# Kernel tuning notes

Hardware: AMD Instinct MI355X
Metric: run time of the kernel (lower is better)

## Reference

```python
import jax, jax.numpy as jnp
import numpy as np

B, S, D, H, L = 64, 512, 512, 512, 2


def gru_cell(x, h, Wih, Whh, bih, bhh):
    # PyTorch GRUCell math: gates ordered (r, z, n)
    gi = x @ Wih.T + bih          # [B, 3H]
    gh = h @ Whh.T + bhh          # [B, 3H]
    ir, iz, i_n = jnp.split(gi, 3, axis=-1)
    hr, hz, h_n = jnp.split(gh, 3, axis=-1)
    r = jax.nn.sigmoid(ir + hr)
    z = jax.nn.sigmoid(iz + hz)
    n = jnp.tanh(i_n + r * h_n)
    return (1.0 - z) * n + z * h


def setup_inputs() -> dict:
    key = jax.random.key(0)
    ks = jax.random.split(key, 12)
    s = 0.05
    inp = {
        "input": jax.random.normal(ks[0], (B, S, D), jnp.float32),
        "encoder_h": jax.random.normal(ks[1], (L, B, 2 * H), jnp.float32),
        # stacked per-layer GRUCell params (input_size == hidden_size so layer dims match)
        "Wih_f": jax.random.normal(ks[2], (L, 3 * H, D), jnp.float32) * s,
        "Whh_f": jax.random.normal(ks[3], (L, 3 * H, H), jnp.float32) * s,
        "bih_f": jax.random.normal(ks[4], (L, 3 * H), jnp.float32) * s,
        "bhh_f": jax.random.normal(ks[5], (L, 3 * H), jnp.float32) * s,
        "Wih_b": jax.random.normal(ks[6], (L, 3 * H, D), jnp.float32) * s,
        "Whh_b": jax.random.normal(ks[7], (L, 3 * H, H), jnp.float32) * s,
        "bih_b": jax.random.normal(ks[8], (L, 3 * H), jnp.float32) * s,
        "bhh_b": jax.random.normal(ks[9], (L, 3 * H), jnp.float32) * s,
    }
    return inp


def reference(input, encoder_h, Wih_f, Whh_f, bih_f, bhh_f, Wih_b, Whh_b, bih_b, bhh_b):
    n_layers = Wih_f.shape[0]
    hidden = Whh_f.shape[-1]
    h_f0 = encoder_h[:, :, :hidden]   # [L, B, H]
    h_b0 = encoder_h[:, :, hidden:]   # [L, B, H]
    xs_f = jnp.swapaxes(input, 0, 1)  # [S, B, D]
    xs_b = jnp.flip(xs_f, axis=0)     # reversed sequence

    def step(carry, xt):
        h_f, h_b = carry
        x_f, x_b = xt
        hf_new, hb_new = [], []
        for j in range(n_layers):
            x_f = gru_cell(x_f, h_f[j], Wih_f[j], Whh_f[j], bih_f[j], bhh_f[j])
            x_b = gru_cell(x_b, h_b[j], Wih_b[j], Whh_b[j], bih_b[j], bhh_b[j])
            hf_new.append(x_f)
            hb_new.append(x_b)
        return (jnp.stack(hf_new), jnp.stack(hb_new)), (x_f, x_b)

    (h_f, h_b), (out_f, out_b) = jax.lax.scan(step, (h_f0, h_b0), (xs_f, xs_b))
    out_f = jnp.swapaxes(out_f, 0, 1)                  # [B, S, H]
    out_b = jnp.flip(jnp.swapaxes(out_b, 0, 1), axis=1)  # un-reverse in time
    out = jnp.concatenate([out_f, out_b], axis=-1)      # [B, S, 2H]
    h = jnp.concatenate([h_f, h_b], axis=-1)            # [L, B, 2H]
    return out, h
```

## Files before the change

### kernel.cpp

```cpp
#include <hip/hip_runtime.h>

constexpr int BATCH = 64;
constexpr int SEQ   = 512;
constexpr int DIN   = 512;
constexpr int HID   = 512;
constexpr int LAY   = 2;
constexpr int G3    = 3 * HID;
constexpr int KPAD  = 522;

typedef __attribute__((ext_vector_type(8))) short bf16x8;
typedef __attribute__((ext_vector_type(4))) float f32x4;
typedef unsigned short u16;
typedef unsigned int   u32;
typedef unsigned long long u64;

__device__ __forceinline__ u16 f2bf(float f) {
  union { float f; u32 u; } v; v.f = f;
  return (u16)((v.u + 0x7fffu + ((v.u >> 16) & 1u)) >> 16);
}

__device__ __forceinline__ u64 ld_agent_u64(const u16* p) {
  return __hip_atomic_load((const u64*)p, __ATOMIC_RELAXED, __HIP_MEMORY_SCOPE_AGENT);
}
__device__ __forceinline__ bf16x8 ld_frag_agent(const u16* p) {
  union { u64 q[2]; bf16x8 f; } u;
  u.q[0] = ld_agent_u64(p);
  u.q[1] = ld_agent_u64(p + 4);
  return u.f;
}
__device__ __forceinline__ void st_agent_u16(u16* p, u16 v) {
  __hip_atomic_store(p, v, __ATOMIC_RELAXED, __HIP_MEMORY_SCOPE_AGENT);
}
__device__ __forceinline__ void st_agent_u32(u32* p, u32 v) {
  __hip_atomic_store(p, v, __ATOMIC_RELAXED, __HIP_MEMORY_SCOPE_AGENT);
}

__device__ __forceinline__ void poll_ge(const u32* flags, u32 target) {
  const int idx = threadIdx.x & 31;
  for (;;) {
    u32 v = __hip_atomic_load(flags + idx, __ATOMIC_RELAXED, __HIP_MEMORY_SCOPE_AGENT);
    #pragma unroll
    for (int off = 16; off >= 1; off >>= 1) {
      u32 o = (u32)__shfl_xor((int)v, off, 64);
      v = v < o ? v : o;
    }
    if (v >= target) break;
    __builtin_amdgcn_s_sleep(1);
  }
  __asm__ volatile("" ::: "memory");
}

struct Params {
  const float* input;
  const float* enc_h;
  const float* Wih[2];
  const float* Whh[2];
  const float* bih[2];
  const float* bhh[2];
  float* out;
  u16* xin;
  u16* wih;
  u16* whh;
  u16* out0;
  u16* hbf;
  u32* flags;
};

__global__ __launch_bounds__(256) void convert_kernel(Params p) {
  const int gtid = blockIdx.x * 256 + threadIdx.x;
  const int nthr = gridDim.x * 256;
  for (int i = gtid; i < BATCH * SEQ * DIN; i += nthr) p.xin[i] = f2bf(p.input[i]);
  for (int d = 0; d < 2; ++d) {
    const float* s1 = p.Wih[d];
    u16* d1 = p.wih + (size_t)d * LAY * G3 * DIN;
    for (int i = gtid; i < LAY * G3 * DIN; i += nthr) d1[i] = f2bf(s1[i]);
    const float* s2 = p.Whh[d];
    u16* d2 = p.whh + (size_t)d * LAY * G3 * HID;
    for (int i = gtid; i < LAY * G3 * HID; i += nthr) d2[i] = f2bf(s2[i]);
  }
  if (gtid < LAY * 2 * 32) p.flags[gtid] = 0;
}

__global__ __launch_bounds__(256, 1) void recur_all(Params p) {
  const int wg    = blockIdx.x;
  const int layer = wg >> 6;
  const int cwg   = wg & 63;
  const int dir   = cwg & 1;
  const int slice = cwg >> 1;
  const int j0    = slice * 16;
  const int wave  = threadIdx.x >> 6;
  const int lane  = threadIdx.x & 63;
  const int lq = lane >> 4, ln = lane & 15;
  const int j = j0 + ln;

  __shared__ u16 lwhh[3][16][KPAD];
  {
    const u16* whh = p.whh + ((size_t)dir * LAY + layer) * G3 * HID;
    for (int idx = threadIdx.x; idx < 3 * 16 * 64; idx += 256) {
      const int k8 = idx & 63, row = idx >> 6;
      const int g = row >> 4, jj = row & 15;
      *(bf16x8*)&lwhh[g][jj][k8 * 8] =
          *(const bf16x8*)(whh + (size_t)(g * HID + j0 + jj) * HID + k8 * 8);
    }
  }

  u16* hbL = p.hbf + (size_t)layer * 2 * 2 * BATCH * HID;
  u16* hb[2] = { hbL + (size_t)dir * BATCH * HID,
                 hbL + (size_t)(2 + dir) * BATCH * HID };

  const u16* wih = p.wih + ((size_t)dir * LAY + layer) * G3 * DIN;
  const u16* bri[3];
  #pragma unroll
  for (int g = 0; g < 3; ++g) bri[g] = wih + (size_t)(g * HID + j) * DIN;

  const float* bih = p.bih[dir] + (size_t)layer * G3;
  const float* bhh = p.bhh[dir] + (size_t)layer * G3;
  const float b_r  = bih[j] + bhh[j];
  const float b_z  = bih[HID + j] + bhh[HID + j];
  const float bi_n = bih[2 * HID + j];
  const float bh_n = bhh[2 * HID + j];

  float hreg[4];
  #pragma unroll
  for (int i = 0; i < 4; ++i) {
    const int m = wave * 16 + lq * 4 + i;
    hreg[i] = p.enc_h[((size_t)layer * BATCH + m) * (2 * HID) + (size_t)dir * HID + j];
    st_agent_u16(&hb[0][(size_t)m * HID + j], f2bf(hreg[i]));
  }

  u32* fown  = p.flags + (size_t)(layer * 2 + dir) * 32;
  u32* fdep  = p.flags + (size_t)dir * 32;
  u32* fslot = fown + slice;

  __threadfence_block();
  __syncthreads();
  if (threadIdx.x == 0) st_agent_u32(fslot, 1);

  const int am = wave * 16 + ln;
  float* hsec = p.out + (size_t)BATCH * SEQ * 2 * HID;

  f32x4 accx[3];
  if (layer == 1) poll_ge(fdep, 2);
  {
    const u16* ax = (layer == 0)
        ? p.xin + ((size_t)am * SEQ + (dir ? SEQ - 1 : 0)) * DIN
        : p.out0 + ((size_t)dir * SEQ * BATCH + am) * HID;
    accx[0] = f32x4{0, 0, 0, 0}; accx[1] = accx[0]; accx[2] = accx[0];
    #pragma unroll 4
    for (int k0 = 0; k0 < 512; k0 += 32) {
      const int koff = k0 + lq * 8;
      const bf16x8 a_x = (layer == 0) ? *(const bf16x8*)(ax + koff)
                                      : ld_frag_agent(ax + koff);
      #pragma unroll
      for (int g = 0; g < 3; ++g)
        accx[g] = __builtin_amdgcn_mfma_f32_16x16x32_bf16(
            a_x, *(const bf16x8*)(bri[g] + koff), accx[g], 0, 0, 0);
    }
  }
  poll_ge(fown, 1);

  for (int t = 0; t < SEQ; ++t) {
    const u16* ah = hb[t & 1] + (size_t)am * HID;
    f32x4 acch[3] = {};
    #pragma unroll 4
    for (int k0 = 0; k0 < 512; k0 += 32) {
      const int koff = k0 + lq * 8;
      const bf16x8 a_h = ld_frag_agent(ah + koff);
      #pragma unroll
      for (int g = 0; g < 3; ++g)
        acch[g] = __builtin_amdgcn_mfma_f32_16x16x32_bf16(
            a_h, *(const bf16x8*)&lwhh[g][ln][koff], acch[g], 0, 0, 0);
    }

    u16* hwrite = hb[(t + 1) & 1];
    #pragma unroll
    for (int i = 0; i < 4; ++i) {
      const int m = wave * 16 + lq * 4 + i;
      const float r = 1.f / (1.f + __expf(-(accx[0][i] + acch[0][i] + b_r)));
      const float z = 1.f / (1.f + __expf(-(accx[1][i] + acch[1][i] + b_z)));
      const float n = tanhf(accx[2][i] + bi_n + r * (acch[2][i] + bh_n));
      const float hnew = (1.f - z) * n + z * hreg[i];
      hreg[i] = hnew;
      if (t + 1 < SEQ) st_agent_u16(&hwrite[(size_t)m * HID + j], f2bf(hnew));
      if (layer == 0) {
        st_agent_u16(&p.out0[(((size_t)dir * SEQ + t) * BATCH + m) * HID + j], f2bf(hnew));
      } else {
        const int tt = dir ? (SEQ - 1 - t) : t;
        p.out[((size_t)m * SEQ + tt) * (2 * HID) + (size_t)dir * HID + j] = hnew;
      }
      if (t == SEQ - 1)
        hsec[((size_t)layer * BATCH + m) * (2 * HID) + (size_t)dir * HID + j] = hnew;
    }

    __threadfence_block();
    __syncthreads();
    if (threadIdx.x == 0) st_agent_u32(fslot, (u32)(t + 2));

    if (t + 1 < SEQ) {
      if (layer == 1) poll_ge(fdep, (u32)(t + 3));
      const int tn = t + 1;
      const u16* ax = (layer == 0)
          ? p.xin + ((size_t)am * SEQ + (dir ? SEQ - 1 - tn : tn)) * DIN
          : p.out0 + (((size_t)dir * SEQ + tn) * BATCH + am) * HID;
      accx[0] = f32x4{0, 0, 0, 0}; accx[1] = accx[0]; accx[2] = accx[0];
      #pragma unroll 4
      for (int k0 = 0; k0 < 512; k0 += 32) {
        const int koff = k0 + lq * 8;
        const bf16x8 a_x = (layer == 0) ? *(const bf16x8*)(ax + koff)
                                        : ld_frag_agent(ax + koff);
        #pragma unroll
        for (int g = 0; g < 3; ++g)
          accx[g] = __builtin_amdgcn_mfma_f32_16x16x32_bf16(
              a_x, *(const bf16x8*)(bri[g] + koff), accx[g], 0, 0, 0);
      }
      poll_ge(fown, (u32)(t + 2));
    }
  }
}

extern "C" void kernel_launch(void* const* d_in, const int* in_sizes, int n_in,
                              void* d_out, int out_size, void* d_ws, size_t ws_size,
                              hipStream_t stream) {
  Params p;
  p.input  = (const float*)d_in[0];
  p.enc_h  = (const float*)d_in[1];
  p.Wih[0] = (const float*)d_in[2];
  p.Whh[0] = (const float*)d_in[3];
  p.bih[0] = (const float*)d_in[4];
  p.bhh[0] = (const float*)d_in[5];
  p.Wih[1] = (const float*)d_in[6];
  p.Whh[1] = (const float*)d_in[7];
  p.bih[1] = (const float*)d_in[8];
  p.bhh[1] = (const float*)d_in[9];
  p.out = (float*)d_out;

  uintptr_t base = (uintptr_t)d_ws;
  size_t off = 0;
  auto take = [&](size_t bytes) -> void* {
    void* r = (void*)(base + off);
    off += (bytes + 255) & ~(size_t)255;
    return r;
  };
  p.xin   = (u16*)take((size_t)BATCH * SEQ * DIN * 2);
  p.wih   = (u16*)take((size_t)2 * LAY * G3 * DIN * 2);
  p.whh   = (u16*)take((size_t)2 * LAY * G3 * HID * 2);
  p.out0  = (u16*)take((size_t)2 * SEQ * BATCH * HID * 2);
  p.hbf   = (u16*)take((size_t)LAY * 2 * 2 * BATCH * HID * 2);
  p.flags = (u32*)take((size_t)LAY * 2 * 32 * 4);
  if (off > ws_size) return;

  convert_kernel<<<dim3(2048), dim3(256), 0, stream>>>(p);
  recur_all<<<dim3(128), dim3(256), 0, stream>>>(p);
}
```

Before: 8.067 ms.

## Halve workgroups with wider hidden slices and switch to atomic-counter barrier

Each workgroup now handles 32 hidden units with 512 threads (8 waves split over batch and output tiles), so 64 workgroups run instead of 128. Per-slice flag arrays with shuffle-min polling are replaced by one atomic fetch-add counter per cell, polled by a single wave and then a block barrier. The recurrent h fragments are preloaded into registers right after the input projection, and the LDS weight tile uses an XOR swizzle instead of padding. The goal is fewer participants in each cross-workgroup sync and lower per-step latency. The cost is higher register pressure, atomic contention on one counter, and an extra __syncthreads per step.

```diff
diff --git a/kernel.cpp b/kernel.cpp
--- a/kernel.cpp
+++ b/kernel.cpp
@@ -6,7 +6,11 @@
 constexpr int HID   = 512;
 constexpr int LAY   = 2;
 constexpr int G3    = 3 * HID;
-constexpr int KPAD  = 522;
+
+constexpr int NSLICE = 16;
+constexpr int WSLICE = 32;
+constexpr int NTHR   = 512;
+constexpr int CNTPAD = 1024;
 
 typedef __attribute__((ext_vector_type(8))) short bf16x8;
 typedef __attribute__((ext_vector_type(4))) float f32x4;
@@ -31,19 +35,10 @@
 __device__ __forceinline__ void st_agent_u16(u16* p, u16 v) {
   __hip_atomic_store(p, v, __ATOMIC_RELAXED, __HIP_MEMORY_SCOPE_AGENT);
 }
-__device__ __forceinline__ void st_agent_u32(u32* p, u32 v) {
-  __hip_atomic_store(p, v, __ATOMIC_RELAXED, __HIP_MEMORY_SCOPE_AGENT);
-}
-
-__device__ __forceinline__ void poll_ge(const u32* flags, u32 target) {
-  const int idx = threadIdx.x & 31;
+
+__device__ __forceinline__ void poll1(const u32* c, u32 target) {
   for (;;) {
-    u32 v = __hip_atomic_load(flags + idx, __ATOMIC_RELAXED, __HIP_MEMORY_SCOPE_AGENT);
-    #pragma unroll
-    for (int off = 16; off >= 1; off >>= 1) {
-      u32 o = (u32)__shfl_xor((int)v, off, 64);
-      v = v < o ? v : o;
-    }
+    u32 v = __hip_atomic_load(c, __ATOMIC_RELAXED, __HIP_MEMORY_SCOPE_AGENT);
     if (v >= target) break;
     __builtin_amdgcn_s_sleep(1);
   }
@@ -63,7 +58,7 @@
   u16* whh;
   u16* out0;
   u16* hbf;
-  u32* flags;
+  u32* cnt;
 };
 
 __global__ __launch_bounds__(256) void convert_kernel(Params p) {
@@ -78,35 +73,39 @@
     u16* d2 = p.whh + (size_t)d * LAY * G3 * HID;
     for (int i = gtid; i < LAY * G3 * HID; i += nthr) d2[i] = f2bf(s2[i]);
   }
-  if (gtid < LAY * 2 * 32) p.flags[gtid] = 0;
-}
-
-__global__ __launch_bounds__(256, 1) void recur_all(Params p) {
+  if (gtid < 4 * CNTPAD) p.cnt[gtid] = 0;
+}
+
+__global__ __launch_bounds__(NTHR, 1) void recur_all(Params p) {
   const int wg    = blockIdx.x;
-  const int layer = wg >> 6;
-  const int cwg   = wg & 63;
-  const int dir   = cwg & 1;
-  const int slice = cwg >> 1;
-  const int j0    = slice * 16;
-  const int wave  = threadIdx.x >> 6;
-  const int lane  = threadIdx.x & 63;
+  const int cell  = wg & 3;
+  const int layer = cell >> 1;
+  const int dir   = cell & 1;
+  const int slice = wg >> 2;
+  const int j0    = slice * WSLICE;
+
+  const int wave = threadIdx.x >> 6;
+  const int lane = threadIdx.x & 63;
   const int lq = lane >> 4, ln = lane & 15;
-  const int j = j0 + ln;
-
-  __shared__ u16 lwhh[3][16][KPAD];
+  const int mt = wave & 3, nt = wave >> 2;
+  const int am = mt * 16 + ln;
+  const int rr = nt * 16 + ln;
+  const int j  = j0 + rr;
+
+  __shared__ u16 lwhh[3][WSLICE][512];
   {
     const u16* whh = p.whh + ((size_t)dir * LAY + layer) * G3 * HID;
-    for (int idx = threadIdx.x; idx < 3 * 16 * 64; idx += 256) {
+    for (int idx = threadIdx.x; idx < 3 * WSLICE * 64; idx += NTHR) {
       const int k8 = idx & 63, row = idx >> 6;
-      const int g = row >> 4, jj = row & 15;
-      *(bf16x8*)&lwhh[g][jj][k8 * 8] =
+      const int g = row >> 5, jj = row & 31;
+      *(bf16x8*)&lwhh[g][jj][(k8 ^ (jj & 7)) * 8] =
           *(const bf16x8*)(whh + (size_t)(g * HID + j0 + jj) * HID + k8 * 8);
     }
   }
 
   u16* hbL = p.hbf + (size_t)layer * 2 * 2 * BATCH * HID;
-  u16* hb[2] = { hbL + (size_t)dir * BATCH * HID,
-                 hbL + (size_t)(2 + dir) * BATCH * HID };
+  u16* hb0 = hbL + (size_t)dir * BATCH * HID;
+  u16* hb1 = hbL + (size_t)(2 + dir) * BATCH * HID;
 
   const u16* wih = p.wih + ((size_t)dir * LAY + layer) * G3 * DIN;
   const u16* bri[3];
@@ -123,59 +122,70 @@
   float hreg[4];
   #pragma unroll
   for (int i = 0; i < 4; ++i) {
-    const int m = wave * 16 + lq * 4 + i;
+    const int m = mt * 16 + lq * 4 + i;
     hreg[i] = p.enc_h[((size_t)layer * BATCH + m) * (2 * HID) + (size_t)dir * HID + j];
-    st_agent_u16(&hb[0][(size_t)m * HID + j], f2bf(hreg[i]));
-  }
-
-  u32* fown  = p.flags + (size_t)(layer * 2 + dir) * 32;
-  u32* fdep  = p.flags + (size_t)dir * 32;
-  u32* fslot = fown + slice;
+    st_agent_u16(&hb0[(size_t)m * HID + j], f2bf(hreg[i]));
+  }
+
+  u32* own = p.cnt + (size_t)cell * CNTPAD;
+  u32* dep = p.cnt + (size_t)dir  * CNTPAD;
 
   __threadfence_block();
   __syncthreads();
-  if (threadIdx.x == 0) st_agent_u32(fslot, 1);
-
-  const int am = wave * 16 + ln;
+  if (threadIdx.x == 0)
+    __hip_atomic_fetch_add(own, 1u, __ATOMIC_RELAXED, __HIP_MEMORY_SCOPE_AGENT);
+
   float* hsec = p.out + (size_t)BATCH * SEQ * 2 * HID;
 
-  f32x4 accx[3];
-  if (layer == 1) poll_ge(fdep, 2);
+  bf16x8 fr[16];
+  f32x4  accx[3];
+
+  if (layer == 1) { if (wave == 0) poll1(dep, 2 * NSLICE); __syncthreads(); }
   {
     const u16* ax = (layer == 0)
         ? p.xin + ((size_t)am * SEQ + (dir ? SEQ - 1 : 0)) * DIN
         : p.out0 + ((size_t)dir * SEQ * BATCH + am) * HID;
-    accx[0] = f32x4{0, 0, 0, 0}; accx[1] = accx[0]; accx[2] = accx[0];
-    #pragma unroll 4
-    for (int k0 = 0; k0 < 512; k0 += 32) {
-      const int koff = k0 + lq * 8;
-      const bf16x8 a_x = (layer == 0) ? *(const bf16x8*)(ax + koff)
-                                      : ld_frag_agent(ax + koff);
-      #pragma unroll
-      for (int g = 0; g < 3; ++g)
-        accx[g] = __builtin_amdgcn_mfma_f32_16x16x32_bf16(
-            a_x, *(const bf16x8*)(bri[g] + koff), accx[g], 0, 0, 0);
-    }
-  }
-  poll_ge(fown, 1);
+    if (layer == 0) {
+      #pragma unroll
+      for (int kk = 0; kk < 16; ++kk) fr[kk] = *(const bf16x8*)(ax + kk * 32 + lq * 8);
+    } else {
+      #pragma unroll
+      for (int kk = 0; kk < 16; ++kk) fr[kk] = ld_frag_agent(ax + kk * 32 + lq * 8);
+    }
+  }
+  if (wave == 0) poll1(own, NSLICE);
+  __syncthreads();
+  accx[0] = f32x4{0.f, 0.f, 0.f, 0.f}; accx[1] = accx[0]; accx[2] = accx[0];
+  #pragma unroll
+  for (int kk = 0; kk < 16; ++kk) {
+    #pragma unroll
+    for (int g = 0; g < 3; ++g)
+      accx[g] = __builtin_amdgcn_mfma_f32_16x16x32_bf16(
+          fr[kk], *(const bf16x8*)(bri[g] + kk * 32 + lq * 8), accx[g], 0, 0, 0);
+  }
+  {
+    const u16* ah = hb0 + (size_t)am * HID;
+    #pragma unroll
+    for (int kk = 0; kk < 16; ++kk) fr[kk] = ld_frag_agent(ah + kk * 32 + lq * 8);
+  }
 
   for (int t = 0; t < SEQ; ++t) {
-    const u16* ah = hb[t & 1] + (size_t)am * HID;
-    f32x4 acch[3] = {};
-    #pragma unroll 4
-    for (int k0 = 0; k0 < 512; k0 += 32) {
-      const int koff = k0 + lq * 8;
-      const bf16x8 a_h = ld_frag_agent(ah + koff);
+    f32x4 acch[3];
+    acch[0] = f32x4{0.f, 0.f, 0.f, 0.f}; acch[1] = acch[0]; acch[2] = acch[0];
+    #pragma unroll
+    for (int kk = 0; kk < 16; ++kk) {
       #pragma unroll
       for (int g = 0; g < 3; ++g)
         acch[g] = __builtin_amdgcn_mfma_f32_16x16x32_bf16(
-            a_h, *(const bf16x8*)&lwhh[g][ln][koff], acch[g], 0, 0, 0);
-    }
-
-    u16* hwrite = hb[(t + 1) & 1];
+            fr[kk],
+            *(const bf16x8*)&lwhh[g][rr][(((kk << 2) + lq) ^ (rr & 7)) * 8],
+            acch[g], 0, 0, 0);
+    }
+
+    u16* hwrite = ((t + 1) & 1) ? hb1 : hb0;
     #pragma unroll
     for (int i = 0; i < 4; ++i) {
-      const int m = wave * 16 + lq * 4 + i;
+      const int m = mt * 16 + lq * 4 + i;
       const float r = 1.f / (1.f + __expf(-(accx[0][i] + acch[0][i] + b_r)));
       const float z = 1.f / (1.f + __expf(-(accx[1][i] + acch[1][i] + b_z)));
       const float n = tanhf(accx[2][i] + bi_n + r * (acch[2][i] + bh_n));
@@ -194,26 +204,35 @@
 
     __threadfence_block();
     __syncthreads();
-    if (threadIdx.x == 0) st_agent_u32(fslot, (u32)(t + 2));
+    if (threadIdx.x == 0)
+      __hip_atomic_fetch_add(own, 1u, __ATOMIC_RELAXED, __HIP_MEMORY_SCOPE_AGENT);
 
     if (t + 1 < SEQ) {
-      if (layer == 1) poll_ge(fdep, (u32)(t + 3));
       const int tn = t + 1;
+      if (layer == 1) { if (wave == 0) poll1(dep, (u32)(NSLICE * (tn + 2))); __syncthreads(); }
       const u16* ax = (layer == 0)
           ? p.xin + ((size_t)am * SEQ + (dir ? SEQ - 1 - tn : tn)) * DIN
           : p.out0 + (((size_t)dir * SEQ + tn) * BATCH + am) * HID;
-      accx[0] = f32x4{0, 0, 0, 0}; accx[1] = accx[0]; accx[2] = accx[0];
-      #pragma unroll 4
-      for (int k0 = 0; k0 < 512; k0 += 32) {
-        const int koff = k0 + lq * 8;
-        const bf16x8 a_x = (layer == 0) ? *(const bf16x8*)(ax + koff)
-                                        : ld_frag_agent(ax + koff);
+      if (layer == 0) {
+        #pragma unroll
+        for (int kk = 0; kk < 16; ++kk) fr[kk] = *(const bf16x8*)(ax + kk * 32 + lq * 8);
+      } else {
+        #pragma unroll
+        for (int kk = 0; kk < 16; ++kk) fr[kk] = ld_frag_agent(ax + kk * 32 + lq * 8);
+      }
+      if (wave == 0) poll1(own, (u32)(NSLICE * (t + 2)));
+      __syncthreads();
+      accx[0] = f32x4{0.f, 0.f, 0.f, 0.f}; accx[1] = accx[0]; accx[2] = accx[0];
+      #pragma unroll
+      for (int kk = 0; kk < 16; ++kk) {
         #pragma unroll
         for (int g = 0; g < 3; ++g)
           accx[g] = __builtin_amdgcn_mfma_f32_16x16x32_bf16(
-              a_x, *(const bf16x8*)(bri[g] + koff), accx[g], 0, 0, 0);
+              fr[kk], *(const bf16x8*)(bri[g] + kk * 32 + lq * 8), accx[g], 0, 0, 0);
       }
-      poll_ge(fown, (u32)(t + 2));
+      const u16* ah = ((tn & 1) ? hb1 : hb0) + (size_t)am * HID;
+      #pragma unroll
+      for (int kk = 0; kk < 16; ++kk) fr[kk] = ld_frag_agent(ah + kk * 32 + lq * 8);
     }
   }
 }
@@ -246,9 +265,9 @@
   p.whh   = (u16*)take((size_t)2 * LAY * G3 * HID * 2);
   p.out0  = (u16*)take((size_t)2 * SEQ * BATCH * HID * 2);
   p.hbf   = (u16*)take((size_t)LAY * 2 * 2 * BATCH * HID * 2);
-  p.flags = (u32*)take((size_t)LAY * 2 * 32 * 4);
+  p.cnt   = (u32*)take((size_t)4 * CNTPAD * 4);
   if (off > ws_size) return;
 
   convert_kernel<<<dim3(2048), dim3(256), 0, stream>>>(p);
-  recur_all<<<dim3(128), dim3(256), 0, stream>>>(p);
-}
+  recur_all<<<dim3(64), dim3(NTHR), 0, stream>>>(p);
+}
```

New measurement: 13.43 ms. 1.66x slower.

## Fuse both GRU layers into one wavefront-skewed workgroup per slice

Applied to the files above, without the earlier changes.

Each workgroup now computes both layers for its hidden slice and direction. Layer 1 runs one timestep behind layer 0, so one step's layer-0 hidden-state fragment serves both the layer-0 recurrent GEMM and the layer-1 input GEMM. This removes the separate layer-1 workgroups, the out0 staging buffer and the cross-layer flag polling, and halves the grid from 128 to 64 workgroups. In exchange each workgroup does roughly twice the serial MFMA work per step with half the parallelism, and holds both layers' Whh slices in LDS.

```diff
diff --git a/kernel.cpp b/kernel.cpp
--- a/kernel.cpp
+++ b/kernel.cpp
@@ -61,7 +61,6 @@
   u16* xin;
   u16* wih;
   u16* whh;
-  u16* out0;
   u16* hbf;
   u32* flags;
 };
@@ -78,142 +77,182 @@
     u16* d2 = p.whh + (size_t)d * LAY * G3 * HID;
     for (int i = gtid; i < LAY * G3 * HID; i += nthr) d2[i] = f2bf(s2[i]);
   }
-  if (gtid < LAY * 2 * 32) p.flags[gtid] = 0;
+  if (gtid < 2 * 32) p.flags[gtid] = 0;
 }
 
 __global__ __launch_bounds__(256, 1) void recur_all(Params p) {
   const int wg    = blockIdx.x;
-  const int layer = wg >> 6;
-  const int cwg   = wg & 63;
-  const int dir   = cwg & 1;
-  const int slice = cwg >> 1;
+  const int dir   = wg & 1;
+  const int slice = wg >> 1;
   const int j0    = slice * 16;
   const int wave  = threadIdx.x >> 6;
   const int lane  = threadIdx.x & 63;
   const int lq = lane >> 4, ln = lane & 15;
-  const int j = j0 + ln;
-
-  __shared__ u16 lwhh[3][16][KPAD];
+  const int j  = j0 + ln;
+  const int am = wave * 16 + ln;
+
+  __shared__ u16 lwhh[LAY][3][16][KPAD];
   {
-    const u16* whh = p.whh + ((size_t)dir * LAY + layer) * G3 * HID;
-    for (int idx = threadIdx.x; idx < 3 * 16 * 64; idx += 256) {
+    const u16* whh = p.whh + (size_t)dir * LAY * G3 * HID;
+    for (int idx = threadIdx.x; idx < LAY * 3 * 16 * 64; idx += 256) {
       const int k8 = idx & 63, row = idx >> 6;
-      const int g = row >> 4, jj = row & 15;
-      *(bf16x8*)&lwhh[g][jj][k8 * 8] =
-          *(const bf16x8*)(whh + (size_t)(g * HID + j0 + jj) * HID + k8 * 8);
-    }
-  }
-
-  u16* hbL = p.hbf + (size_t)layer * 2 * 2 * BATCH * HID;
-  u16* hb[2] = { hbL + (size_t)dir * BATCH * HID,
-                 hbL + (size_t)(2 + dir) * BATCH * HID };
-
-  const u16* wih = p.wih + ((size_t)dir * LAY + layer) * G3 * DIN;
-  const u16* bri[3];
+      const int lay = row >= 48;
+      const int rem = row - lay * 48;
+      const int g = rem >> 4, jj = rem & 15;
+      *(bf16x8*)&lwhh[lay][g][jj][k8 * 8] =
+          *(const bf16x8*)(whh + ((size_t)lay * G3 + (size_t)(g * HID + j0 + jj)) * HID + k8 * 8);
+    }
+  }
+
+  u16* h0b[2], * h1b[2];
   #pragma unroll
-  for (int g = 0; g < 3; ++g) bri[g] = wih + (size_t)(g * HID + j) * DIN;
-
-  const float* bih = p.bih[dir] + (size_t)layer * G3;
-  const float* bhh = p.bhh[dir] + (size_t)layer * G3;
-  const float b_r  = bih[j] + bhh[j];
-  const float b_z  = bih[HID + j] + bhh[HID + j];
-  const float bi_n = bih[2 * HID + j];
-  const float bh_n = bhh[2 * HID + j];
-
-  float hreg[4];
+  for (int par = 0; par < 2; ++par) {
+    h0b[par] = p.hbf + ((size_t)(0 * 2 + par) * 2 + dir) * BATCH * HID;
+    h1b[par] = p.hbf + ((size_t)(1 * 2 + par) * 2 + dir) * BATCH * HID;
+  }
+
+  const u16* wih = p.wih + (size_t)dir * LAY * G3 * DIN;
+  const u16* bri0[3];
+  const u16* bri1[3];
+  #pragma unroll
+  for (int g = 0; g < 3; ++g) {
+    bri0[g] = wih + (size_t)(g * HID + j) * DIN;
+    bri1[g] = wih + ((size_t)G3 + (size_t)(g * HID + j)) * DIN;
+  }
+
+  const float* bih0 = p.bih[dir];
+  const float* bhh0 = p.bhh[dir];
+  const float* bih1 = bih0 + G3;
+  const float* bhh1 = bhh0 + G3;
+  const float b0_r  = bih0[j] + bhh0[j];
+  const float b0_z  = bih0[HID + j] + bhh0[HID + j];
+  const float b0_in = bih0[2 * HID + j];
+  const float b0_hn = bhh0[2 * HID + j];
+  const float b1_r  = bih1[j] + bhh1[j];
+  const float b1_z  = bih1[HID + j] + bhh1[HID + j];
+  const float b1_in = bih1[2 * HID + j];
+  const float b1_hn = bhh1[2 * HID + j];
+
+  float hreg0[4], hreg1[4];
   #pragma unroll
   for (int i = 0; i < 4; ++i) {
     const int m = wave * 16 + lq * 4 + i;
-    hreg[i] = p.enc_h[((size_t)layer * BATCH + m) * (2 * HID) + (size_t)dir * HID + j];
-    st_agent_u16(&hb[0][(size_t)m * HID + j], f2bf(hreg[i]));
-  }
-
-  u32* fown  = p.flags + (size_t)(layer * 2 + dir) * 32;
-  u32* fdep  = p.flags + (size_t)dir * 32;
+    hreg0[i] = p.enc_h[(size_t)m * (2 * HID) + (size_t)dir * HID + j];
+    st_agent_u16(&h0b[0][(size_t)m * HID + j], f2bf(hreg0[i]));
+    hreg1[i] = p.enc_h[((size_t)BATCH + m) * (2 * HID) + (size_t)dir * HID + j];
+    st_agent_u16(&h1b[0][(size_t)m * HID + j], f2bf(hreg1[i]));
+  }
+
+  u32* fown  = p.flags + (size_t)dir * 32;
   u32* fslot = fown + slice;
 
   __threadfence_block();
   __syncthreads();
   if (threadIdx.x == 0) st_agent_u32(fslot, 1);
 
-  const int am = wave * 16 + ln;
   float* hsec = p.out + (size_t)BATCH * SEQ * 2 * HID;
 
-  f32x4 accx[3];
-  if (layer == 1) poll_ge(fdep, 2);
+  f32x4 accx0[3];
+  accx0[0] = f32x4{0, 0, 0, 0}; accx0[1] = accx0[0]; accx0[2] = accx0[0];
   {
-    const u16* ax = (layer == 0)
-        ? p.xin + ((size_t)am * SEQ + (dir ? SEQ - 1 : 0)) * DIN
-        : p.out0 + ((size_t)dir * SEQ * BATCH + am) * HID;
-    accx[0] = f32x4{0, 0, 0, 0}; accx[1] = accx[0]; accx[2] = accx[0];
+    const u16* ax = p.xin + ((size_t)am * SEQ + (dir ? SEQ - 1 : 0)) * DIN;
     #pragma unroll 4
     for (int k0 = 0; k0 < 512; k0 += 32) {
       const int koff = k0 + lq * 8;
-      const bf16x8 a_x = (layer == 0) ? *(const bf16x8*)(ax + koff)
-                                      : ld_frag_agent(ax + koff);
-      #pragma unroll
-      for (int g = 0; g < 3; ++g)
-        accx[g] = __builtin_amdgcn_mfma_f32_16x16x32_bf16(
-            a_x, *(const bf16x8*)(bri[g] + koff), accx[g], 0, 0, 0);
+      const bf16x8 a_x = *(const bf16x8*)(ax + koff);
+      #pragma unroll
+      for (int g = 0; g < 3; ++g)
+        accx0[g] = __builtin_amdgcn_mfma_f32_16x16x32_bf16(
+            a_x, *(const bf16x8*)(bri0[g] + koff), accx0[g], 0, 0, 0);
     }
   }
   poll_ge(fown, 1);
 
-  for (int t = 0; t < SEQ; ++t) {
-    const u16* ah = hb[t & 1] + (size_t)am * HID;
-    f32x4 acch[3] = {};
+  for (int i = 0; i <= SEQ; ++i) {
+    const u16* h0r = h0b[i & 1] + (size_t)am * HID;
+    const u16* h1r = h1b[(i + 1) & 1] + (size_t)am * HID;
+    f32x4 acch0[3], accx1[3], acch1[3];
+    acch0[0] = f32x4{0, 0, 0, 0}; acch0[1] = acch0[0]; acch0[2] = acch0[0];
+    accx1[0] = acch0[0]; accx1[1] = acch0[0]; accx1[2] = acch0[0];
+    acch1[0] = acch0[0]; acch1[1] = acch0[0]; acch1[2] = acch0[0];
     #pragma unroll 4
     for (int k0 = 0; k0 < 512; k0 += 32) {
       const int koff = k0 + lq * 8;
-      const bf16x8 a_h = ld_frag_agent(ah + koff);
-      #pragma unroll
-      for (int g = 0; g < 3; ++g)
-        acch[g] = __builtin_amdgcn_mfma_f32_16x16x32_bf16(
-            a_h, *(const bf16x8*)&lwhh[g][ln][koff], acch[g], 0, 0, 0);
-    }
-
-    u16* hwrite = hb[(t + 1) & 1];
-    #pragma unroll
-    for (int i = 0; i < 4; ++i) {
-      const int m = wave * 16 + lq * 4 + i;
-      const float r = 1.f / (1.f + __expf(-(accx[0][i] + acch[0][i] + b_r)));
-      const float z = 1.f / (1.f + __expf(-(accx[1][i] + acch[1][i] + b_z)));
-      const float n = tanhf(accx[2][i] + bi_n + r * (acch[2][i] + bh_n));
-      const float hnew = (1.f - z) * n + z * hreg[i];
-      hreg[i] = hnew;
-      if (t + 1 < SEQ) st_agent_u16(&hwrite[(size_t)m * HID + j], f2bf(hnew));
-      if (layer == 0) {
-        st_agent_u16(&p.out0[(((size_t)dir * SEQ + t) * BATCH + m) * HID + j], f2bf(hnew));
-      } else {
-        const int tt = dir ? (SEQ - 1 - t) : t;
+      const bf16x8 a0 = ld_frag_agent(h0r + koff);
+      #pragma unroll
+      for (int g = 0; g < 3; ++g)
+        acch0[g] = __builtin_amdgcn_mfma_f32_16x16x32_bf16(
+            a0, *(const bf16x8*)&lwhh[0][g][ln][koff], acch0[g], 0, 0, 0);
+      #pragma unroll
+      for (int g = 0; g < 3; ++g)
+        accx1[g] = __builtin_amdgcn_mfma_f32_16x16x32_bf16(
+            a0, *(const bf16x8*)(bri1[g] + koff), accx1[g], 0, 0, 0);
+    }
+    #pragma unroll 4
+    for (int k0 = 0; k0 < 512; k0 += 32) {
+      const int koff = k0 + lq * 8;
+      const bf16x8 a1 = ld_frag_agent(h1r + koff);
+      #pragma unroll
+      for (int g = 0; g < 3; ++g)
+        acch1[g] = __builtin_amdgcn_mfma_f32_16x16x32_bf16(
+            a1, *(const bf16x8*)&lwhh[1][g][ln][koff], acch1[g], 0, 0, 0);
+    }
+
+    if (i < SEQ) {
+      u16* hw = h0b[(i + 1) & 1];
+      #pragma unroll
+      for (int r = 0; r < 4; ++r) {
+        const int m = wave * 16 + lq * 4 + r;
+        const float rg = 1.f / (1.f + __expf(-(accx0[0][r] + acch0[0][r] + b0_r)));
+        const float zg = 1.f / (1.f + __expf(-(accx0[1][r] + acch0[1][r] + b0_z)));
+        const float ng = tanhf(accx0[2][r] + b0_in + rg * (acch0[2][r] + b0_hn));
+        const float hnew = (1.f - zg) * ng + zg * hreg0[r];
+        hreg0[r] = hnew;
+        st_agent_u16(&hw[(size_t)m * HID + j], f2bf(hnew));
+        if (i == SEQ - 1)
+          hsec[(size_t)m * (2 * HID) + (size_t)dir * HID + j] = hnew;
+      }
+    }
+
+    if (i >= 1) {
+      const int t  = i - 1;
+      const int tt = dir ? (SEQ - 1 - t) : t;
+      u16* hw = h1b[i & 1];
+      #pragma unroll
+      for (int r = 0; r < 4; ++r) {
+        const int m = wave * 16 + lq * 4 + r;
+        const float rg = 1.f / (1.f + __expf(-(accx1[0][r] + acch1[0][r] + b1_r)));
+        const float zg = 1.f / (1.f + __expf(-(accx1[1][r] + acch1[1][r] + b1_z)));
+        const float ng = tanhf(accx1[2][r] + b1_in + rg * (acch1[2][r] + b1_hn));
+        const float hnew = (1.f - zg) * ng + zg * hreg1[r];
+        hreg1[r] = hnew;
+        if (i < SEQ) st_agent_u16(&hw[(size_t)m * HID + j], f2bf(hnew));
         p.out[((size_t)m * SEQ + tt) * (2 * HID) + (size_t)dir * HID + j] = hnew;
+        if (i == SEQ)
+          hsec[((size_t)BATCH + m) * (2 * HID) + (size_t)dir * HID + j] = hnew;
       }
-      if (t == SEQ - 1)
-        hsec[((size_t)layer * BATCH + m) * (2 * HID) + (size_t)dir * HID + j] = hnew;
     }
 
     __threadfence_block();
     __syncthreads();
-    if (threadIdx.x == 0) st_agent_u32(fslot, (u32)(t + 2));
-
-    if (t + 1 < SEQ) {
-      if (layer == 1) poll_ge(fdep, (u32)(t + 3));
-      const int tn = t + 1;
-      const u16* ax = (layer == 0)
-          ? p.xin + ((size_t)am * SEQ + (dir ? SEQ - 1 - tn : tn)) * DIN
-          : p.out0 + (((size_t)dir * SEQ + tn) * BATCH + am) * HID;
-      accx[0] = f32x4{0, 0, 0, 0}; accx[1] = accx[0]; accx[2] = accx[0];
-      #pragma unroll 4
-      for (int k0 = 0; k0 < 512; k0 += 32) {
-        const int koff = k0 + lq * 8;
-        const bf16x8 a_x = (layer == 0) ? *(const bf16x8*)(ax + koff)
-                                        : ld_frag_agent(ax + koff);
-        #pragma unroll
-        for (int g = 0; g < 3; ++g)
-          accx[g] = __builtin_amdgcn_mfma_f32_16x16x32_bf16(
-              a_x, *(const bf16x8*)(bri[g] + koff), accx[g], 0, 0, 0);
+    if (threadIdx.x == 0) st_agent_u32(fslot, (u32)(i + 2));
+
+    if (i < SEQ) {
+      if (i + 1 < SEQ) {
+        const int tn = i + 1;
+        const u16* ax = p.xin + ((size_t)am * SEQ + (dir ? SEQ - 1 - tn : tn)) * DIN;
+        accx0[0] = f32x4{0, 0, 0, 0}; accx0[1] = accx0[0]; accx0[2] = accx0[0];
+        #pragma unroll 4
+        for (int k0 = 0; k0 < 512; k0 += 32) {
+          const int koff = k0 + lq * 8;
+          const bf16x8 a_x = *(const bf16x8*)(ax + koff);
+          #pragma unroll
+          for (int g = 0; g < 3; ++g)
+            accx0[g] = __builtin_amdgcn_mfma_f32_16x16x32_bf16(
+                a_x, *(const bf16x8*)(bri0[g] + koff), accx0[g], 0, 0, 0);
+        }
       }
-      poll_ge(fown, (u32)(t + 2));
+      poll_ge(fown, (u32)(i + 2));
     }
   }
 }
@@ -244,11 +283,10 @@
   p.xin   = (u16*)take((size_t)BATCH * SEQ * DIN * 2);
   p.wih   = (u16*)take((size_t)2 * LAY * G3 * DIN * 2);
   p.whh   = (u16*)take((size_t)2 * LAY * G3 * HID * 2);
-  p.out0  = (u16*)take((size_t)2 * SEQ * BATCH * HID * 2);
   p.hbf   = (u16*)take((size_t)LAY * 2 * 2 * BATCH * HID * 2);
-  p.flags = (u32*)take((size_t)LAY * 2 * 32 * 4);
+  p.flags = (u32*)take((size_t)2 * 32 * 4);
   if (off > ws_size) return;
 
   convert_kernel<<<dim3(2048), dim3(256), 0, stream>>>(p);
-  recur_all<<<dim3(128), dim3(256), 0, stream>>>(p);
-}
+  recur_all<<<dim3(64), dim3(256), 0, stream>>>(p);
+}
```

Result: slower. 11.88 ms (+47.3%).

## Pin each GRU cell to one XCC and use L2-local flag and state exchange

Applied to the files above, without the earlier changes.

Work groups are grouped so that each (layer, direction) cell's 16 work groups come from the same blockIdx&7 class. At startup each work group reads its hardware XCC id, and the group checks whether all 16 landed on the same XCC. When they did, the per-step hidden state and progress flags are exchanged through plain stores and sc0 loads that stay coherent within that XCC's L2, instead of device-scope atomics. Each work group now covers 32 hidden columns instead of 16, which halves the number of synchronizing work groups per cell. Layer 0 also reads its recurrent state straight from the out0 time slots, so it no longer keeps a separate double buffer. The cost is that half of the launched blocks exit immediately, each active block does twice the MFMA work per step, and correctness depends on the XCC placement check.

```diff
diff --git a/kernel.cpp b/kernel.cpp
--- a/kernel.cpp
+++ b/kernel.cpp
@@ -6,7 +6,9 @@
 constexpr int HID   = 512;
 constexpr int LAY   = 2;
 constexpr int G3    = 3 * HID;
-constexpr int KPAD  = 522;
+constexpr int WCOL  = 32;
+constexpr int KPAD  = 520;
+constexpr int SLOTS = SEQ + 1;
 
 typedef __attribute__((ext_vector_type(8))) short bf16x8;
 typedef __attribute__((ext_vector_type(4))) float f32x4;
@@ -35,16 +37,30 @@
   __hip_atomic_store(p, v, __ATOMIC_RELAXED, __HIP_MEMORY_SCOPE_AGENT);
 }
 
-__device__ __forceinline__ void poll_ge(const u32* flags, u32 target) {
-  const int idx = threadIdx.x & 31;
+__device__ __forceinline__ u32 min16(u32 v) {
+  #pragma unroll
+  for (int off = 8; off >= 1; off >>= 1) {
+    u32 o = (u32)__shfl_xor((int)v, off, 64);
+    v = v < o ? v : o;
+  }
+  return v;
+}
+__device__ __forceinline__ void poll16_agent(const u32* f, u32 tgt) {
+  const int idx = threadIdx.x & 15;
   for (;;) {
-    u32 v = __hip_atomic_load(flags + idx, __ATOMIC_RELAXED, __HIP_MEMORY_SCOPE_AGENT);
-    #pragma unroll
-    for (int off = 16; off >= 1; off >>= 1) {
-      u32 o = (u32)__shfl_xor((int)v, off, 64);
-      v = v < o ? v : o;
-    }
-    if (v >= target) break;
+    u32 v = __hip_atomic_load(f + idx, __ATOMIC_RELAXED, __HIP_MEMORY_SCOPE_AGENT);
+    if (min16(v) >= tgt) break;
+    __builtin_amdgcn_s_sleep(1);
+  }
+  __asm__ volatile("" ::: "memory");
+}
+__device__ __forceinline__ void poll16_sc0(const u32* f, u32 tgt) {
+  const u32* p = f + (threadIdx.x & 15);
+  for (;;) {
+    u32 v;
+    asm volatile("global_load_dword %0, %1, off sc0\n\ts_waitcnt vmcnt(0)"
+                 : "=v"(v) : "v"(p) : "memory");
+    if (min16(v) >= tgt) break;
     __builtin_amdgcn_s_sleep(1);
   }
   __asm__ volatile("" ::: "memory");
@@ -78,142 +94,217 @@
     u16* d2 = p.whh + (size_t)d * LAY * G3 * HID;
     for (int i = gtid; i < LAY * G3 * HID; i += nthr) d2[i] = f2bf(s2[i]);
   }
-  if (gtid < LAY * 2 * 32) p.flags[gtid] = 0;
+  if (gtid < 4096) p.flags[gtid] = 0;
 }
 
 __global__ __launch_bounds__(256, 1) void recur_all(Params p) {
-  const int wg    = blockIdx.x;
-  const int layer = wg >> 6;
-  const int cwg   = wg & 63;
-  const int dir   = cwg & 1;
-  const int slice = cwg >> 1;
-  const int j0    = slice * 16;
+  const int cls = blockIdx.x & 7;
+  if (cls >= 4) return;
+  const int cell  = cls;
+  const int layer = cell >> 1;
+  const int dir   = cell & 1;
+  const int slice = blockIdx.x >> 3;
+  const int j0    = slice * WCOL;
   const int wave  = threadIdx.x >> 6;
   const int lane  = threadIdx.x & 63;
   const int lq = lane >> 4, ln = lane & 15;
-  const int j = j0 + ln;
-
-  __shared__ u16 lwhh[3][16][KPAD];
+  const int am = wave * 16 + ln;
+
+  __shared__ u16 lwhh[3][WCOL][KPAD];
+  __shared__ int s_local;
+
   {
     const u16* whh = p.whh + ((size_t)dir * LAY + layer) * G3 * HID;
-    for (int idx = threadIdx.x; idx < 3 * 16 * 64; idx += 256) {
+    for (int idx = threadIdx.x; idx < 3 * WCOL * 64; idx += 256) {
       const int k8 = idx & 63, row = idx >> 6;
-      const int g = row >> 4, jj = row & 15;
-      *(bf16x8*)&lwhh[g][jj][k8 * 8] =
-          *(const bf16x8*)(whh + (size_t)(g * HID + j0 + jj) * HID + k8 * 8);
-    }
-  }
-
-  u16* hbL = p.hbf + (size_t)layer * 2 * 2 * BATCH * HID;
-  u16* hb[2] = { hbL + (size_t)dir * BATCH * HID,
-                 hbL + (size_t)(2 + dir) * BATCH * HID };
+      const int g = row >> 5, rr = row & 31;
+      *(bf16x8*)&lwhh[g][rr][k8 * 8] =
+          *(const bf16x8*)(whh + (size_t)(g * HID + j0 + rr) * HID + k8 * 8);
+    }
+  }
+
+  {
+    const u32 xcc = (u32)__builtin_amdgcn_s_getreg(63508);
+    u32* xarr = p.flags + 2048 + (size_t)cell * 64;
+    if (threadIdx.x == 0) {
+      st_agent_u32(xarr + slice, xcc + 1);
+      for (;;) {
+        bool all = true, uni = true; u32 r0 = 0;
+        for (int i = 0; i < 16; ++i) {
+          u32 v = __hip_atomic_load(xarr + i, __ATOMIC_RELAXED, __HIP_MEMORY_SCOPE_AGENT);
+          if (i == 0) r0 = v;
+          all = all && (v != 0);
+          uni = uni && (v == r0);
+        }
+        if (all) { s_local = uni ? 1 : 0; break; }
+        __builtin_amdgcn_s_sleep(8);
+      }
+    }
+    __syncthreads();
+  }
+  const bool local = (s_local != 0);
+
+  u16* o0 = p.out0 + (size_t)dir * SLOTS * BATCH * HID;
+  u16* hbp[2] = { p.hbf + ((size_t)cell * 2 + 0) * BATCH * HID,
+                  p.hbf + ((size_t)cell * 2 + 1) * BATCH * HID };
+  u32* fown = p.flags + (size_t)cell * 64;
+  u32* fdep = p.flags + 1024 + (size_t)dir * 64;
 
   const u16* wih = p.wih + ((size_t)dir * LAY + layer) * G3 * DIN;
-  const u16* bri[3];
-  #pragma unroll
-  for (int g = 0; g < 3; ++g) bri[g] = wih + (size_t)(g * HID + j) * DIN;
+  const u16* bri[3][2];
+  #pragma unroll
+  for (int g = 0; g < 3; ++g)
+    #pragma unroll
+    for (int s = 0; s < 2; ++s)
+      bri[g][s] = wih + (size_t)(g * HID + j0 + s * 16 + ln) * DIN;
 
   const float* bih = p.bih[dir] + (size_t)layer * G3;
   const float* bhh = p.bhh[dir] + (size_t)layer * G3;
-  const float b_r  = bih[j] + bhh[j];
-  const float b_z  = bih[HID + j] + bhh[HID + j];
-  const float bi_n = bih[2 * HID + j];
-  const float bh_n = bhh[2 * HID + j];
-
-  float hreg[4];
-  #pragma unroll
-  for (int i = 0; i < 4; ++i) {
-    const int m = wave * 16 + lq * 4 + i;
-    hreg[i] = p.enc_h[((size_t)layer * BATCH + m) * (2 * HID) + (size_t)dir * HID + j];
-    st_agent_u16(&hb[0][(size_t)m * HID + j], f2bf(hreg[i]));
-  }
-
-  u32* fown  = p.flags + (size_t)(layer * 2 + dir) * 32;
-  u32* fdep  = p.flags + (size_t)dir * 32;
-  u32* fslot = fown + slice;
+  float b_r[2], b_z[2], bi_n[2], bh_n[2];
+  #pragma unroll
+  for (int s = 0; s < 2; ++s) {
+    const int jc = j0 + s * 16 + ln;
+    b_r[s]  = bih[jc] + bhh[jc];
+    b_z[s]  = bih[HID + jc] + bhh[HID + jc];
+    bi_n[s] = bih[2 * HID + jc];
+    bh_n[s] = bhh[2 * HID + jc];
+  }
+
+  float hreg[2][4];
+  #pragma unroll
+  for (int s = 0; s < 2; ++s)
+    #pragma unroll
+    for (int i = 0; i < 4; ++i) {
+      const int m = wave * 16 + lq * 4 + i;
+      const int jc = j0 + s * 16 + ln;
+      hreg[s][i] = p.enc_h[((size_t)layer * BATCH + m) * (2 * HID) + (size_t)dir * HID + jc];
+      const u16 h16 = f2bf(hreg[s][i]);
+      const size_t off = (size_t)m * HID + jc;
+      if (local) hbp[0][off] = h16;
+      else if (layer == 1) st_agent_u16(&hbp[0][off], h16);
+      if (layer == 0) st_agent_u16(&o0[off], h16);
+    }
 
   __threadfence_block();
   __syncthreads();
-  if (threadIdx.x == 0) st_agent_u32(fslot, 1);
-
-  const int am = wave * 16 + ln;
+  if (threadIdx.x == 0) {
+    if (local) { fown[slice] = 1; __asm__ volatile("" ::: "memory"); }
+    else st_agent_u32(&fown[slice], 1);
+    if (layer == 0) st_agent_u32(&fdep[slice], 1);
+  }
+
   float* hsec = p.out + (size_t)BATCH * SEQ * 2 * HID;
 
-  f32x4 accx[3];
-  if (layer == 1) poll_ge(fdep, 2);
+  f32x4 accx[3][2];
+  #pragma unroll
+  for (int g = 0; g < 3; ++g) { accx[g][0] = f32x4{0,0,0,0}; accx[g][1] = accx[g][0]; }
+  if (layer == 1) poll16_agent(fdep, 2);
   {
     const u16* ax = (layer == 0)
         ? p.xin + ((size_t)am * SEQ + (dir ? SEQ - 1 : 0)) * DIN
-        : p.out0 + ((size_t)dir * SEQ * BATCH + am) * HID;
-    accx[0] = f32x4{0, 0, 0, 0}; accx[1] = accx[0]; accx[2] = accx[0];
+        : o0 + (size_t)1 * BATCH * HID + (size_t)am * HID;
     #pragma unroll 4
     for (int k0 = 0; k0 < 512; k0 += 32) {
       const int koff = k0 + lq * 8;
-      const bf16x8 a_x = (layer == 0) ? *(const bf16x8*)(ax + koff)
-                                      : ld_frag_agent(ax + koff);
+      const bf16x8 a_x = *(const bf16x8*)(ax + koff);
       #pragma unroll
       for (int g = 0; g < 3; ++g)
-        accx[g] = __builtin_amdgcn_mfma_f32_16x16x32_bf16(
-            a_x, *(const bf16x8*)(bri[g] + koff), accx[g], 0, 0, 0);
-    }
-  }
-  poll_ge(fown, 1);
+        #pragma unroll
+        for (int s = 0; s < 2; ++s)
+          accx[g][s] = __builtin_amdgcn_mfma_f32_16x16x32_bf16(
+              a_x, *(const bf16x8*)(bri[g][s] + koff), accx[g][s], 0, 0, 0);
+    }
+  }
+  if (local) poll16_sc0(fown, 1); else poll16_agent(fown, 1);
 
   for (int t = 0; t < SEQ; ++t) {
-    const u16* ah = hb[t & 1] + (size_t)am * HID;
-    f32x4 acch[3] = {};
-    #pragma unroll 4
-    for (int k0 = 0; k0 < 512; k0 += 32) {
-      const int koff = k0 + lq * 8;
-      const bf16x8 a_h = ld_frag_agent(ah + koff);
+    bf16x8 fh[16];
+    const u16* hsrc = (local || layer == 1)
+        ? hbp[t & 1] + (size_t)am * HID
+        : o0 + (size_t)t * BATCH * HID + (size_t)am * HID;
+    if (local) {
+      #pragma unroll
+      for (int kk = 0; kk < 16; ++kk)
+        asm volatile("global_load_dwordx4 %0, %1, off sc0"
+                     : "=v"(fh[kk]) : "v"(hsrc + kk * 32 + lq * 8));
+      asm volatile("s_waitcnt vmcnt(0)" ::: "memory");
+      __builtin_amdgcn_sched_barrier(0);
+    } else if (layer == 0) {
+      #pragma unroll
+      for (int kk = 0; kk < 16; ++kk) fh[kk] = *(const bf16x8*)(hsrc + kk * 32 + lq * 8);
+    } else {
+      #pragma unroll
+      for (int kk = 0; kk < 16; ++kk) fh[kk] = ld_frag_agent(hsrc + kk * 32 + lq * 8);
+    }
+
+    f32x4 acch[3][2];
+    #pragma unroll
+    for (int g = 0; g < 3; ++g) { acch[g][0] = f32x4{0,0,0,0}; acch[g][1] = acch[g][0]; }
+    #pragma unroll
+    for (int kk = 0; kk < 16; ++kk) {
+      const int koff = kk * 32 + lq * 8;
       #pragma unroll
       for (int g = 0; g < 3; ++g)
-        acch[g] = __builtin_amdgcn_mfma_f32_16x16x32_bf16(
-            a_h, *(const bf16x8*)&lwhh[g][ln][koff], acch[g], 0, 0, 0);
-    }
-
-    u16* hwrite = hb[(t + 1) & 1];
-    #pragma unroll
-    for (int i = 0; i < 4; ++i) {
-      const int m = wave * 16 + lq * 4 + i;
-      const float r = 1.f / (1.f + __expf(-(accx[0][i] + acch[0][i] + b_r)));
-      const float z = 1.f / (1.f + __expf(-(accx[1][i] + acch[1][i] + b_z)));
-      const float n = tanhf(accx[2][i] + bi_n + r * (acch[2][i] + bh_n));
-      const float hnew = (1.f - z) * n + z * hreg[i];
-      hreg[i] = hnew;
-      if (t + 1 < SEQ) st_agent_u16(&hwrite[(size_t)m * HID + j], f2bf(hnew));
-      if (layer == 0) {
-        st_agent_u16(&p.out0[(((size_t)dir * SEQ + t) * BATCH + m) * HID + j], f2bf(hnew));
-      } else {
-        const int tt = dir ? (SEQ - 1 - t) : t;
-        p.out[((size_t)m * SEQ + tt) * (2 * HID) + (size_t)dir * HID + j] = hnew;
+        #pragma unroll
+        for (int s = 0; s < 2; ++s)
+          acch[g][s] = __builtin_amdgcn_mfma_f32_16x16x32_bf16(
+              fh[kk], *(const bf16x8*)&lwhh[g][s * 16 + ln][koff], acch[g][s], 0, 0, 0);
+    }
+
+    u16* hw = hbp[(t + 1) & 1];
+    u16* ow = o0 + (size_t)(t + 1) * BATCH * HID;
+    const int tt = dir ? (SEQ - 1 - t) : t;
+    #pragma unroll
+    for (int s = 0; s < 2; ++s)
+      #pragma unroll
+      for (int i = 0; i < 4; ++i) {
+        const int m = wave * 16 + lq * 4 + i;
+        const int jc = j0 + s * 16 + ln;
+        const float r = 1.f / (1.f + __expf(-(accx[0][s][i] + acch[0][s][i] + b_r[s])));
+        const float z = 1.f / (1.f + __expf(-(accx[1][s][i] + acch[1][s][i] + b_z[s])));
+        const float n = tanhf(accx[2][s][i] + bi_n[s] + r * (acch[2][s][i] + bh_n[s]));
+        const float hnew = (1.f - z) * n + z * hreg[s][i];
+        hreg[s][i] = hnew;
+        const u16 h16 = f2bf(hnew);
+        const size_t off = (size_t)m * HID + jc;
+        if (t + 1 < SEQ) {
+          if (local) hw[off] = h16;
+          else if (layer == 1) st_agent_u16(&hw[off], h16);
+        }
+        if (layer == 0) st_agent_u16(&ow[off], h16);
+        else p.out[((size_t)m * SEQ + tt) * (2 * HID) + (size_t)dir * HID + jc] = hnew;
+        if (t == SEQ - 1)
+          hsec[((size_t)layer * BATCH + m) * (2 * HID) + (size_t)dir * HID + jc] = hnew;
       }
-      if (t == SEQ - 1)
-        hsec[((size_t)layer * BATCH + m) * (2 * HID) + (size_t)dir * HID + j] = hnew;
-    }
 
     __threadfence_block();
     __syncthreads();
-    if (threadIdx.x == 0) st_agent_u32(fslot, (u32)(t + 2));
+    if (threadIdx.x == 0) {
+      if (local) { fown[slice] = (u32)(t + 2); __asm__ volatile("" ::: "memory"); }
+      else st_agent_u32(&fown[slice], (u32)(t + 2));
+      if (layer == 0) st_agent_u32(&fdep[slice], (u32)(t + 2));
+    }
 
     if (t + 1 < SEQ) {
-      if (layer == 1) poll_ge(fdep, (u32)(t + 3));
+      if (layer == 1) poll16_agent(fdep, (u32)(t + 3));
       const int tn = t + 1;
       const u16* ax = (layer == 0)
           ? p.xin + ((size_t)am * SEQ + (dir ? SEQ - 1 - tn : tn)) * DIN
-          : p.out0 + (((size_t)dir * SEQ + tn) * BATCH + am) * HID;
-      accx[0] = f32x4{0, 0, 0, 0}; accx[1] = accx[0]; accx[2] = accx[0];
+          : o0 + (size_t)(tn + 1) * BATCH * HID + (size_t)am * HID;
+      #pragma unroll
+      for (int g = 0; g < 3; ++g) { accx[g][0] = f32x4{0,0,0,0}; accx[g][1] = accx[g][0]; }
       #pragma unroll 4
       for (int k0 = 0; k0 < 512; k0 += 32) {
         const int koff = k0 + lq * 8;
-        const bf16x8 a_x = (layer == 0) ? *(const bf16x8*)(ax + koff)
-                                        : ld_frag_agent(ax + koff);
+        const bf16x8 a_x = *(const bf16x8*)(ax + koff);
         #pragma unroll
         for (int g = 0; g < 3; ++g)
-          accx[g] = __builtin_amdgcn_mfma_f32_16x16x32_bf16(
-              a_x, *(const bf16x8*)(bri[g] + koff), accx[g], 0, 0, 0);
+          #pragma unroll
+          for (int s = 0; s < 2; ++s)
+            accx[g][s] = __builtin_amdgcn_mfma_f32_16x16x32_bf16(
+                a_x, *(const bf16x8*)(bri[g][s] + koff), accx[g][s], 0, 0, 0);
       }
-      poll_ge(fown, (u32)(t + 2));
+      if (local) poll16_sc0(fown, (u32)(t + 2)); else poll16_agent(fown, (u32)(t + 2));
     }
   }
 }
@@ -244,9 +335,9 @@
   p.xin   = (u16*)take((size_t)BATCH * SEQ * DIN * 2);
   p.wih   = (u16*)take((size_t)2 * LAY * G3 * DIN * 2);
   p.whh   = (u16*)take((size_t)2 * LAY * G3 * HID * 2);
-  p.out0  = (u16*)take((size_t)2 * SEQ * BATCH * HID * 2);
-  p.hbf   = (u16*)take((size_t)LAY * 2 * 2 * BATCH * HID * 2);
-  p.flags = (u32*)take((size_t)LAY * 2 * 32 * 4);
+  p.out0  = (u16*)take((size_t)2 * SLOTS * BATCH * HID * 2);
+  p.hbf   = (u16*)take((size_t)4 * 2 * BATCH * HID * 2);
+  p.flags = (u32*)take((size_t)4096 * 4);
   if (off > ws_size) return;
 
   convert_kernel<<<dim3(2048), dim3(256), 0, stream>>>(p);
```

After: 9.587 ms. 18.8% more time.
